# Optimization experiments

Measured on AMD Instinct MI355X. Metric: run time of the kernel, lower is better.

Reference implementation:

```python
import jax, jax.numpy as jnp
import numpy as np

T, B, D, H, O = 64, 64, 512, 512, 128

def setup_inputs() -> dict:
    key = jax.random.key(0)
    ks = jax.random.split(key, 8)
    s = 0.05
    return {
        "x": jax.random.normal(ks[0], (T, B, D), jnp.float32),
        "w_ih": jax.random.normal(ks[1], (T, 4 * H, D), jnp.float32) * s,
        "w_hh": jax.random.normal(ks[2], (T, 4 * H, H), jnp.float32) * s,
        "b_ih": jax.random.normal(ks[3], (T, 4 * H), jnp.float32) * s,
        "b_hh": jax.random.normal(ks[4], (T, 4 * H), jnp.float32) * s,
        "w_ho": jax.random.normal(ks[5], (O, H), jnp.float32) * s,
        "b_ho": jax.random.normal(ks[6], (O,), jnp.float32) * s,
        "lengths": jax.random.randint(ks[7], (B,), 1, T + 1, jnp.int64 if jax.config.jax_enable_x64 else jnp.int32),
    }

def _lstm_scan(x, w_ih, w_hh, b_ih, b_hh):
    bs = x.shape[1]
    h0 = jnp.zeros((bs, H), x.dtype)
    c0 = jnp.zeros((bs, H), x.dtype)

    def step(carry, inp):
        h, c = carry
        xt, Wih, Whh, bih, bhh = inp
        # gates: [B, 4H], torch gate order i, f, g, o
        gates = xt @ Wih.T + bih + h @ Whh.T + bhh
        i, f, g, o = jnp.split(gates, 4, axis=-1)
        c = jax.nn.sigmoid(f) * c + jax.nn.sigmoid(i) * jnp.tanh(g)
        h = jax.nn.sigmoid(o) * jnp.tanh(c)
        return (h, c), h

    (_, _), outs = jax.lax.scan(step, (h0, c0), (x, w_ih, w_hh, b_ih, b_hh))
    return outs  # [T, B, H]

def reference(x, w_ih, w_hh, b_ih, b_hh, w_ho, b_ho, lengths):
    outs = _lstm_scan(x, w_ih, w_hh, b_ih, b_hh)
    bs = x.shape[1]
    h_t = outs[lengths - 1, jnp.arange(bs)]  # [B, H] last valid output per seq
    logits = h_t @ w_ho.T + b_ho
    return jax.nn.log_softmax(logits, axis=1)
```

## Files before the change

### kernel.cpp

```cpp
#include <hip/hip_runtime.h>
#include <math.h>

#define TT 64
#define BB 64
#define DD 512
#define HH 512
#define G4 2048
#define OO 128

typedef unsigned short us16;
typedef __attribute__((ext_vector_type(8))) short bf16x8;
typedef __attribute__((ext_vector_type(4))) float f32x4;
typedef __attribute__((ext_vector_type(4))) unsigned u32x4;

__device__ __forceinline__ unsigned pk_bf16(float lo, float hi) {
  unsigned r;
  asm volatile("v_cvt_pk_bf16_f32 %0, %1, %2" : "=v"(r) : "v"(lo), "v"(hi));
  return r;
}

__device__ __forceinline__ float sigm(float v) { return 1.f / (1.f + expf(-v)); }

__device__ __forceinline__ u32x4 load_b128_cc(const void* p) {
  u32x4 r;
  asm volatile("global_load_dwordx4 %0, %1, off sc0 sc1" : "=v"(r) : "v"(p));
  return r;
}
__device__ __forceinline__ void store_b128_cc(void* p, u32x4 v) {
  asm volatile("global_store_dwordx4 %0, %1, off sc0 sc1" ::"v"(p), "v"(v) : "memory");
}

__global__ __launch_bounds__(256) void phaseA_mfma(
    const float* __restrict__ x, const float* __restrict__ wih,
    const float* __restrict__ bih, const float* __restrict__ bhh,
    float* __restrict__ Gb) {
  __shared__ us16 xa[2][64][64];
  __shared__ us16 wbuf[2][128][64];
  const int tid = threadIdx.x;
  const int t = blockIdx.y;
  const int j0 = blockIdx.x * 128;
  const int wv = tid >> 6, lane = tid & 63;
  const int wm = wv & 1, wn = wv >> 1;
  const float* xb = x + (size_t)t * (BB * DD);
  const float* wg = wih + (size_t)t * (G4 * DD) + (size_t)j0 * DD;

  float4 xr[2][2], wr[4][2];
  int xrow[2], xc[2], wrow[4], wc[4];
#pragma unroll
  for (int i = 0; i < 2; i++) { int cid = tid + i * 256; xrow[i] = cid >> 3; xc[i] = cid & 7; }
#pragma unroll
  for (int i = 0; i < 4; i++) { int cid = tid + i * 256; wrow[i] = cid >> 3; wc[i] = cid & 7; }

  auto loadx = [&](int k0) {
#pragma unroll
    for (int i = 0; i < 2; i++) {
      const float* p = xb + xrow[i] * DD + k0 + xc[i] * 8;
      xr[i][0] = *(const float4*)p; xr[i][1] = *(const float4*)(p + 4);
    }
  };
  auto loadw = [&](int k0) {
#pragma unroll
    for (int i = 0; i < 4; i++) {
      const float* p = wg + (size_t)wrow[i] * DD + k0 + wc[i] * 8;
      wr[i][0] = *(const float4*)p; wr[i][1] = *(const float4*)(p + 4);
    }
  };
  auto store = [&](int buf) {
#pragma unroll
    for (int i = 0; i < 2; i++) {
      uint4 u;
      u.x = pk_bf16(xr[i][0].x, xr[i][0].y); u.y = pk_bf16(xr[i][0].z, xr[i][0].w);
      u.z = pk_bf16(xr[i][1].x, xr[i][1].y); u.w = pk_bf16(xr[i][1].z, xr[i][1].w);
      int p = xc[i] ^ (xrow[i] & 7);
      *(uint4*)&xa[buf][xrow[i]][p * 8] = u;
    }
#pragma unroll
    for (int i = 0; i < 4; i++) {
      uint4 u;
      u.x = pk_bf16(wr[i][0].x, wr[i][0].y); u.y = pk_bf16(wr[i][0].z, wr[i][0].w);
      u.z = pk_bf16(wr[i][1].x, wr[i][1].y); u.w = pk_bf16(wr[i][1].z, wr[i][1].w);
      int p = wc[i] ^ (wrow[i] & 7);
      *(uint4*)&wbuf[buf][wrow[i]][p * 8] = u;
    }
  };

  loadx(0); loadw(0); store(0);
  __syncthreads();

  f32x4 zero = {0.f, 0.f, 0.f, 0.f};
  f32x4 acc[2][4];
#pragma unroll
  for (int mt = 0; mt < 2; mt++)
#pragma unroll
    for (int nt = 0; nt < 4; nt++) acc[mt][nt] = zero;

  for (int s = 0; s < 8; s++) {
    const int nb = s & 1;
    if (s < 7) { loadx((s + 1) * 64); loadw((s + 1) * 64); }
#pragma unroll
    for (int ks = 0; ks < 2; ks++) {
      const int cc = ks * 4 + (lane >> 4);
      bf16x8 a[2], b[4];
#pragma unroll
      for (int mt = 0; mt < 2; mt++) {
        int r = wm * 32 + mt * 16 + (lane & 15);
        a[mt] = *(const bf16x8*)&xa[nb][r][(cc ^ (r & 7)) * 8];
      }
#pragma unroll
      for (int nt = 0; nt < 4; nt++) {
        int r = wn * 64 + nt * 16 + (lane & 15);
        b[nt] = *(const bf16x8*)&wbuf[nb][r][(cc ^ (r & 7)) * 8];
      }
#pragma unroll
      for (int mt = 0; mt < 2; mt++)
#pragma unroll
        for (int nt = 0; nt < 4; nt++)
          acc[mt][nt] = __builtin_amdgcn_mfma_f32_16x16x32_bf16(a[mt], b[nt], acc[mt][nt], 0, 0, 0);
    }
    __syncthreads();
    if (s < 7) store(nb ^ 1);
    __syncthreads();
  }

  float bias[4]; int jn[4];
#pragma unroll
  for (int nt = 0; nt < 4; nt++) {
    jn[nt] = j0 + wn * 64 + nt * 16 + (lane & 15);
    bias[nt] = bih[t * G4 + jn[nt]] + bhh[t * G4 + jn[nt]];
  }
#pragma unroll
  for (int mt = 0; mt < 2; mt++)
#pragma unroll
    for (int nt = 0; nt < 4; nt++)
#pragma unroll
      for (int e = 0; e < 4; e++) {
        int brow = wm * 32 + mt * 16 + (lane >> 4) * 4 + e;
        Gb[((size_t)t * BB + brow) * G4 + jn[nt]] = acc[mt][nt][e] + bias[nt];
      }
}

__global__ __launch_bounds__(256, 1) void lstm_persist(
    const float* __restrict__ whh, const float* __restrict__ Gb,
    const int* __restrict__ lengths, char* __restrict__ hb,
    float* __restrict__ hf) {
  __shared__ float gm[2][16][36];

  const int tid = threadIdx.x, bid = blockIdx.x;
  const int bh = bid & 1, ug = bid >> 1;
  const int wv = tid >> 6, lane = tid & 63;
  const int wm = wv & 1, kq = wv >> 1;
  const int l15 = lane & 15, klg = lane >> 4;

  const size_t jrow = (size_t)((l15 >> 2) * 512 + ug * 4 + (l15 & 3));

  float4 pf[8][2];
  auto prefW = [&](int tt) {
    const float* wt = whh + (size_t)tt * (G4 * HH) + jrow * HH;
#pragma unroll
    for (int s = 0; s < 8; s++) {
      const float* p = wt + (size_t)(kq * 32 + s * 4 + klg) * 8;
      pf[s][0] = *(const float4*)p;
      pf[s][1] = *(const float4*)(p + 4);
    }
  };
  bf16x8 wfrag[8];
  auto cvtW = [&]() {
#pragma unroll
    for (int s = 0; s < 8; s++) {
      uint4 u;
      u.x = pk_bf16(pf[s][0].x, pf[s][0].y); u.y = pk_bf16(pf[s][0].z, pf[s][0].w);
      u.z = pk_bf16(pf[s][1].x, pf[s][1].y); u.w = pk_bf16(pf[s][1].z, pf[s][1].w);
      wfrag[s] = __builtin_bit_cast(bf16x8, u);
    }
  };

  float2 gpre[4];
  auto prefG = [&](int tt) {
    if (wv == 0) {
      const float* gbp =
          Gb + ((size_t)tt * BB + bh * 32 + (lane & 31)) * G4 + ug * 4 + ((lane >> 5) << 1);
#pragma unroll
      for (int q = 0; q < 4; q++) gpre[q] = *(const float2*)(gbp + q * 512);
    }
  };

  const size_t cbase =
      (size_t)bh * 65536 + ((size_t)(kq * 64 + klg * 2) * 32 + wm * 16 + l15) * 16;
  const size_t pbase = (size_t)bh * 65536 + ((size_t)ug * 32 + (lane & 31)) * 16;

  const int mylen = (wv == 0) ? lengths[bh * 32 + (lane & 31)] : -2;
  float cst[2] = {0.f, 0.f};

  prefW(0);
  prefG(0);

  for (int t = 0; t < TT; t++) {
    cvtW();

    u32x4 r0[8], r1[8];
    if (t == 0) {
      u32x4 z = {0u, 0u, 0u, 0u};
#pragma unroll
      for (int s = 0; s < 8; s++) { r0[s] = z; r1[s] = z; }
    } else {
      const char* sbase = hb + (size_t)(t & 1) * 131072 + cbase;
      const unsigned tg = (unsigned)t;
      bool ok;
      do {
#pragma unroll
        for (int s = 0; s < 8; s++) {
          r0[s] = load_b128_cc(sbase + (size_t)s * 4096);
          r1[s] = load_b128_cc(sbase + (size_t)s * 4096 + 512);
        }
        asm volatile("s_waitcnt vmcnt(0)" ::: "memory");
        __builtin_amdgcn_sched_barrier(0);
        ok = true;
#pragma unroll
        for (int s = 0; s < 8; s++) ok = ok && (r0[s].z == tg) && (r1[s].z == tg);
      } while (!__all(ok));
    }

    f32x4 acc = {0.f, 0.f, 0.f, 0.f};
#pragma unroll
    for (int s = 0; s < 8; s++) {
      u32x4 fa;
      fa.x = r0[s].x; fa.y = r0[s].y; fa.z = r1[s].x; fa.w = r1[s].y;
      acc = __builtin_amdgcn_mfma_f32_16x16x32_bf16(__builtin_bit_cast(bf16x8, fa),
                                                    wfrag[s], acc, 0, 0, 0);
    }
    *(f32x4*)&gm[kq][l15][wm * 16 + klg * 4] = acc;

    __syncthreads();

    float2 gcur[4];
    if (wv == 0) {
#pragma unroll
      for (int q = 0; q < 4; q++) gcur[q] = gpre[q];
    }
    if (t + 1 < TT) { prefW(t + 1); prefG(t + 1); }

    if (wv == 0) {
      const int b = lane & 31, hi = lane >> 5;
      float hv[2];
#pragma unroll
      for (int uu = 0; uu < 2; uu++) {
        const int lu = hi * 2 + uu;
        float vi = (uu ? gcur[0].y : gcur[0].x) + gm[0][0 + lu][b] + gm[1][0 + lu][b];
        float vf = (uu ? gcur[1].y : gcur[1].x) + gm[0][4 + lu][b] + gm[1][4 + lu][b];
        float vg = (uu ? gcur[2].y : gcur[2].x) + gm[0][8 + lu][b] + gm[1][8 + lu][b];
        float vo = (uu ? gcur[3].y : gcur[3].x) + gm[0][12 + lu][b] + gm[1][12 + lu][b];
        float cn = sigm(vf) * cst[uu] + sigm(vi) * tanhf(vg);
        cst[uu] = cn;
        hv[uu] = sigm(vo) * tanhf(cn);
      }
      unsigned hw = pk_bf16(hv[0], hv[1]);
      unsigned other = __shfl_xor(hw, 32);
      if (mylen - 1 == t) {
        float2 o2; o2.x = hv[0]; o2.y = hv[1];
        *(float2*)&hf[(size_t)(bh * 32 + b) * HH + ug * 4 + hi * 2] = o2;
      }
      if (hi == 0 && t + 1 < TT) {
        u32x4 rec;
        rec.x = hw; rec.y = other; rec.z = (unsigned)(t + 1); rec.w = 0u;
        store_b128_cc(hb + (size_t)((t + 1) & 1) * 131072 + pbase, rec);
      }
    }
  }
}

__global__ __launch_bounds__(128) void finalK(const float* __restrict__ hf,
                                              const float* __restrict__ who,
                                              const float* __restrict__ bho,
                                              float* __restrict__ out) {
  int b = blockIdx.x, o = threadIdx.x;
  const float* h = hf + b * HH;
  const float* w = who + o * HH;
  float s = bho[o];
#pragma unroll 4
  for (int k = 0; k < HH; k += 4) {
    float4 hv = *(const float4*)(h + k);
    float4 wv = *(const float4*)(w + k);
    s += hv.x * wv.x + hv.y * wv.y + hv.z * wv.z + hv.w * wv.w;
  }
  __shared__ float red[2];
  __shared__ float red2[2];
  float m = s;
#pragma unroll
  for (int msk = 32; msk; msk >>= 1) m = fmaxf(m, __shfl_xor(m, msk));
  int wave = o >> 6;
  if ((o & 63) == 0) red[wave] = m;
  __syncthreads();
  m = fmaxf(red[0], red[1]);
  float e = expf(s - m);
#pragma unroll
  for (int msk = 32; msk; msk >>= 1) e += __shfl_xor(e, msk);
  if ((o & 63) == 0) red2[wave] = e;
  __syncthreads();
  float sum = red2[0] + red2[1];
  out[b * OO + o] = (s - m) - logf(sum);
}

extern "C" void kernel_launch(void* const* d_in, const int* in_sizes, int n_in,
                              void* d_out, int out_size, void* d_ws, size_t ws_size,
                              hipStream_t stream) {
  const float* x = (const float*)d_in[0];
  const float* wih = (const float*)d_in[1];
  const float* whh = (const float*)d_in[2];
  const float* bih = (const float*)d_in[3];
  const float* bhh = (const float*)d_in[4];
  const float* who = (const float*)d_in[5];
  const float* bho = (const float*)d_in[6];
  const int* lengths = (const int*)d_in[7];
  float* out = (float*)d_out;

  char* ws = (char*)d_ws;
  float* Gb = (float*)ws;
  char* hb = ws + 33554432;
  float* hf = (float*)(ws + 33554432 + 262144);

  (void)hipMemsetAsync(hb, 0, 262144, stream);

  phaseA_mfma<<<dim3(16, 64), 256, 0, stream>>>(x, wih, bih, bhh, Gb);
  lstm_persist<<<256, 256, 0, stream>>>(whh, Gb, lengths, hb, hf);
  finalK<<<BB, 128, 0, stream>>>(hf, who, bho, out);
}
```

Measured before the change: 342.9 us.

## Use per-block flags and warp-specialized persistent LSTM with LDS weight staging

Replaces the tagged-payload spin on the whole h buffer with per-block flag words polled by two compute waves. It also splits roles across waves: two waves run the MFMA over the full K, one wave does gate math and publishes h, and one wave prefetches and converts the next step's W_hh into double-buffered swizzled LDS. The goal is to shrink polling traffic and take weight loading off the critical recurrence path. In exchange it adds relaxed-atomic flag ordering that relies on s_waitcnt before the flag store, which carries memory-ordering risk.

```diff
diff --git a/kernel.cpp b/kernel.cpp
--- a/kernel.cpp
+++ b/kernel.cpp
@@ -12,6 +12,7 @@
 typedef __attribute__((ext_vector_type(8))) short bf16x8;
 typedef __attribute__((ext_vector_type(4))) float f32x4;
 typedef __attribute__((ext_vector_type(4))) unsigned u32x4;
+typedef __attribute__((ext_vector_type(2))) unsigned u32x2;
 
 __device__ __forceinline__ unsigned pk_bf16(float lo, float hi) {
   unsigned r;
@@ -26,8 +27,8 @@
   asm volatile("global_load_dwordx4 %0, %1, off sc0 sc1" : "=v"(r) : "v"(p));
   return r;
 }
-__device__ __forceinline__ void store_b128_cc(void* p, u32x4 v) {
-  asm volatile("global_store_dwordx4 %0, %1, off sc0 sc1" ::"v"(p), "v"(v) : "memory");
+__device__ __forceinline__ void store_b64_cc(void* p, u32x2 v) {
+  asm volatile("global_store_dwordx2 %0, %1, off sc0 sc1" ::"v"(p), "v"(v) : "memory");
 }
 
 __global__ __launch_bounds__(256) void phaseA_mfma(
@@ -142,113 +143,91 @@
 __global__ __launch_bounds__(256, 1) void lstm_persist(
     const float* __restrict__ whh, const float* __restrict__ Gb,
     const int* __restrict__ lengths, char* __restrict__ hb,
-    float* __restrict__ hf) {
-  __shared__ float gm[2][16][36];
+    float* __restrict__ hf, unsigned* __restrict__ flags) {
+  __shared__ us16 wbuf[2][16][512];
+  __shared__ float gm[16][36];
 
   const int tid = threadIdx.x, bid = blockIdx.x;
   const int bh = bid & 1, ug = bid >> 1;
   const int wv = tid >> 6, lane = tid & 63;
-  const int wm = wv & 1, kq = wv >> 1;
   const int l15 = lane & 15, klg = lane >> 4;
-
-  const size_t jrow = (size_t)((l15 >> 2) * 512 + ug * 4 + (l15 & 3));
-
-  float4 pf[8][2];
-  auto prefW = [&](int tt) {
-    const float* wt = whh + (size_t)tt * (G4 * HH) + jrow * HH;
-#pragma unroll
-    for (int s = 0; s < 8; s++) {
-      const float* p = wt + (size_t)(kq * 32 + s * 4 + klg) * 8;
-      pf[s][0] = *(const float4*)p;
-      pf[s][1] = *(const float4*)(p + 4);
-    }
-  };
-  bf16x8 wfrag[8];
-  auto cvtW = [&]() {
-#pragma unroll
-    for (int s = 0; s < 8; s++) {
-      uint4 u;
-      u.x = pk_bf16(pf[s][0].x, pf[s][0].y); u.y = pk_bf16(pf[s][0].z, pf[s][0].w);
-      u.z = pk_bf16(pf[s][1].x, pf[s][1].y); u.w = pk_bf16(pf[s][1].z, pf[s][1].w);
-      wfrag[s] = __builtin_bit_cast(bf16x8, u);
-    }
-  };
 
   float2 gpre[4];
   auto prefG = [&](int tt) {
-    if (wv == 0) {
-      const float* gbp =
-          Gb + ((size_t)tt * BB + bh * 32 + (lane & 31)) * G4 + ug * 4 + ((lane >> 5) << 1);
-#pragma unroll
-      for (int q = 0; q < 4; q++) gpre[q] = *(const float2*)(gbp + q * 512);
-    }
+    const float* gbp =
+        Gb + ((size_t)tt * BB + bh * 32 + (lane & 31)) * G4 + ug * 4 + ((lane >> 5) << 1);
+#pragma unroll
+    for (int q = 0; q < 4; q++) gpre[q] = *(const float2*)(gbp + q * 512);
   };
-
-  const size_t cbase =
-      (size_t)bh * 65536 + ((size_t)(kq * 64 + klg * 2) * 32 + wm * 16 + l15) * 16;
-  const size_t pbase = (size_t)bh * 65536 + ((size_t)ug * 32 + (lane & 31)) * 16;
-
-  const int mylen = (wv == 0) ? lengths[bh * 32 + (lane & 31)] : -2;
   float cst[2] = {0.f, 0.f};
-
-  prefW(0);
-  prefG(0);
+  const int mylen = (wv == 2) ? lengths[bh * 32 + (lane & 31)] : -2;
+  if (wv == 2) prefG(0);
+
+  float4 pfA[16], pfB[16];
+
+  const char* crb0 = hb + (size_t)bh * 32768 + (size_t)(wv * 16 + l15) * 1024;
 
   for (int t = 0; t < TT; t++) {
-    cvtW();
-
-    u32x4 r0[8], r1[8];
-    if (t == 0) {
-      u32x4 z = {0u, 0u, 0u, 0u};
-#pragma unroll
-      for (int s = 0; s < 8; s++) { r0[s] = z; r1[s] = z; }
-    } else {
-      const char* sbase = hb + (size_t)(t & 1) * 131072 + cbase;
-      const unsigned tg = (unsigned)t;
-      bool ok;
-      do {
-#pragma unroll
-        for (int s = 0; s < 8; s++) {
-          r0[s] = load_b128_cc(sbase + (size_t)s * 4096);
-          r1[s] = load_b128_cc(sbase + (size_t)s * 4096 + 512);
-        }
-        asm volatile("s_waitcnt vmcnt(0)" ::: "memory");
+    if (wv < 2 && t > 0) {
+      const unsigned tgt = (unsigned)t;
+      const int pidx = (2 * (wv * 64 + lane) + bh) * 4;
+      while (true) {
+        unsigned f = __hip_atomic_load(&flags[pidx], __ATOMIC_RELAXED,
+                                       __HIP_MEMORY_SCOPE_AGENT);
+        if (__all(f >= tgt)) break;
+        __builtin_amdgcn_s_sleep(1);
+      }
+    }
+    __builtin_amdgcn_s_barrier();
+    asm volatile("" ::: "memory");
+
+    if (wv < 2) {
+      f32x4 acc = {0.f, 0.f, 0.f, 0.f};
+      if (t > 0) {
+        const char* rb = crb0 + (size_t)(t & 1) * 65536;
+        u32x4 hfrag[16];
+#pragma unroll
+        for (int s = 0; s < 16; s++)
+          hfrag[s] = load_b128_cc(rb + s * 64 + klg * 16);
+        bf16x8 wf[16];
+#pragma unroll
+        for (int s = 0; s < 16; s++)
+          wf[s] = *(const bf16x8*)&wbuf[t & 1][l15][((4 * s + klg) ^ (l15 & 7)) * 8];
+        asm volatile("s_waitcnt vmcnt(0) lgkmcnt(0)" ::: "memory");
         __builtin_amdgcn_sched_barrier(0);
-        ok = true;
-#pragma unroll
-        for (int s = 0; s < 8; s++) ok = ok && (r0[s].z == tg) && (r1[s].z == tg);
-      } while (!__all(ok));
-    }
-
-    f32x4 acc = {0.f, 0.f, 0.f, 0.f};
-#pragma unroll
-    for (int s = 0; s < 8; s++) {
-      u32x4 fa;
-      fa.x = r0[s].x; fa.y = r0[s].y; fa.z = r1[s].x; fa.w = r1[s].y;
-      acc = __builtin_amdgcn_mfma_f32_16x16x32_bf16(__builtin_bit_cast(bf16x8, fa),
-                                                    wfrag[s], acc, 0, 0, 0);
-    }
-    *(f32x4*)&gm[kq][l15][wm * 16 + klg * 4] = acc;
-
-    __syncthreads();
-
-    float2 gcur[4];
-    if (wv == 0) {
+#pragma unroll
+        for (int s = 0; s < 16; s++)
+          acc = __builtin_amdgcn_mfma_f32_16x16x32_bf16(__builtin_bit_cast(bf16x8, hfrag[s]),
+                                                        wf[s], acc, 0, 0, 0);
+      }
+      *(f32x4*)&gm[l15][wv * 16 + klg * 4] = acc;
+      asm volatile("s_waitcnt lgkmcnt(0)" ::: "memory");
+    }
+    if (wv == 3 && t + 1 < TT) {
+      const float* wt = whh + (size_t)(t + 1) * (G4 * HH);
+#pragma unroll
+      for (int j = 0; j < 16; j++) {
+        const float* p = wt + (size_t)((j >> 2) * 512 + ug * 4 + (j & 3)) * HH + lane * 8;
+        pfA[j] = *(const float4*)p;
+        pfB[j] = *(const float4*)(p + 4);
+      }
+    }
+    __builtin_amdgcn_s_barrier();
+    asm volatile("" ::: "memory");
+
+    if (wv == 2) {
+      float2 gcur[4];
 #pragma unroll
       for (int q = 0; q < 4; q++) gcur[q] = gpre[q];
-    }
-    if (t + 1 < TT) { prefW(t + 1); prefG(t + 1); }
-
-    if (wv == 0) {
       const int b = lane & 31, hi = lane >> 5;
       float hv[2];
 #pragma unroll
       for (int uu = 0; uu < 2; uu++) {
         const int lu = hi * 2 + uu;
-        float vi = (uu ? gcur[0].y : gcur[0].x) + gm[0][0 + lu][b] + gm[1][0 + lu][b];
-        float vf = (uu ? gcur[1].y : gcur[1].x) + gm[0][4 + lu][b] + gm[1][4 + lu][b];
-        float vg = (uu ? gcur[2].y : gcur[2].x) + gm[0][8 + lu][b] + gm[1][8 + lu][b];
-        float vo = (uu ? gcur[3].y : gcur[3].x) + gm[0][12 + lu][b] + gm[1][12 + lu][b];
+        float vi = (uu ? gcur[0].y : gcur[0].x) + gm[0 + lu][b];
+        float vf = (uu ? gcur[1].y : gcur[1].x) + gm[4 + lu][b];
+        float vg = (uu ? gcur[2].y : gcur[2].x) + gm[8 + lu][b];
+        float vo = (uu ? gcur[3].y : gcur[3].x) + gm[12 + lu][b];
         float cn = sigm(vf) * cst[uu] + sigm(vi) * tanhf(vg);
         cst[uu] = cn;
         hv[uu] = sigm(vo) * tanhf(cn);
@@ -259,11 +238,30 @@
         float2 o2; o2.x = hv[0]; o2.y = hv[1];
         *(float2*)&hf[(size_t)(bh * 32 + b) * HH + ug * 4 + hi * 2] = o2;
       }
-      if (hi == 0 && t + 1 < TT) {
-        u32x4 rec;
-        rec.x = hw; rec.y = other; rec.z = (unsigned)(t + 1); rec.w = 0u;
-        store_b128_cc(hb + (size_t)((t + 1) & 1) * 131072 + pbase, rec);
-      }
+      if (t + 1 < TT) {
+        if (lane < 32) {
+          u32x2 rec = {hw, other};
+          store_b64_cc(hb + (size_t)((t + 1) & 1) * 65536 + (size_t)bh * 32768 +
+                           (size_t)(lane * 128 + ug) * 8,
+                       rec);
+        }
+        asm volatile("s_waitcnt vmcnt(0)" ::: "memory");
+        if (lane == 0)
+          __hip_atomic_store(&flags[bid * 4], (unsigned)(t + 1), __ATOMIC_RELAXED,
+                             __HIP_MEMORY_SCOPE_AGENT);
+        prefG(t + 1);
+      }
+    }
+    if (wv == 3 && t + 1 < TT) {
+      const int sl = (t + 1) & 1;
+#pragma unroll
+      for (int j = 0; j < 16; j++) {
+        u32x4 w;
+        w.x = pk_bf16(pfA[j].x, pfA[j].y); w.y = pk_bf16(pfA[j].z, pfA[j].w);
+        w.z = pk_bf16(pfB[j].x, pfB[j].y); w.w = pk_bf16(pfB[j].z, pfB[j].w);
+        *(u32x4*)&wbuf[sl][j][(lane ^ (j & 7)) * 8] = w;
+      }
+      asm volatile("s_waitcnt lgkmcnt(0)" ::: "memory");
     }
   }
 }
@@ -316,11 +314,12 @@
   char* ws = (char*)d_ws;
   float* Gb = (float*)ws;
   char* hb = ws + 33554432;
-  float* hf = (float*)(ws + 33554432 + 262144);
-
-  (void)hipMemsetAsync(hb, 0, 262144, stream);
+  unsigned* flags = (unsigned*)(ws + 33554432 + 131072);
+  float* hf = (float*)(ws + 33554432 + 131072 + 4096);
+
+  (void)hipMemsetAsync(flags, 0, 4096, stream);
 
   phaseA_mfma<<<dim3(16, 64), 256, 0, stream>>>(x, wih, bih, bhh, Gb);
-  lstm_persist<<<256, 256, 0, stream>>>(whh, Gb, lengths, hb, hf);
+  lstm_persist<<<256, 256, 0, stream>>>(whh, Gb, lengths, hb, hf, flags);
   finalK<<<BB, 128, 0, stream>>>(hf, who, bho, out);
 }
```

Measured after the change: 418.2 us. 1.22x slower.

## Split persistent LSTM block into compute and weight-prefetch warp roles

Applied to the files above, without the earlier changes.

Warps 0-1 now each handle the full K=512 reduction for 16 batch rows. They read h from the global exchange buffer and W_hh fragments from a swizzled, double-buffered LDS tile. Warps 2-3 act as producers: they load the next timesteps' fp32 W_hh from global, convert it to bf16, and write it into LDS two steps ahead. This removes the per-step cross-warp partial-sum reduction and takes weight loads off the critical path. In exchange, the gate math and h publish are spread across 128 lanes, and a sleep is added in the spin-wait plus priority hints. The risks are that each compute warp now does twice the MFMA chain length, and that the producer/consumer barrier ordering must stay correct.

```diff
diff --git a/kernel.cpp b/kernel.cpp
--- a/kernel.cpp
+++ b/kernel.cpp
@@ -143,127 +143,124 @@
     const float* __restrict__ whh, const float* __restrict__ Gb,
     const int* __restrict__ lengths, char* __restrict__ hb,
     float* __restrict__ hf) {
-  __shared__ float gm[2][16][36];
+  __shared__ us16 wbuf[2][16][512];
+  __shared__ float gmT[2][16][20];
 
   const int tid = threadIdx.x, bid = blockIdx.x;
   const int bh = bid & 1, ug = bid >> 1;
   const int wv = tid >> 6, lane = tid & 63;
-  const int wm = wv & 1, kq = wv >> 1;
   const int l15 = lane & 15, klg = lane >> 4;
 
-  const size_t jrow = (size_t)((l15 >> 2) * 512 + ug * 4 + (l15 & 3));
-
-  float4 pf[8][2];
-  auto prefW = [&](int tt) {
-    const float* wt = whh + (size_t)tt * (G4 * HH) + jrow * HH;
-#pragma unroll
-    for (int s = 0; s < 8; s++) {
-      const float* p = wt + (size_t)(kq * 32 + s * 4 + klg) * 8;
-      pf[s][0] = *(const float4*)p;
-      pf[s][1] = *(const float4*)(p + 4);
-    }
-  };
-  bf16x8 wfrag[8];
-  auto cvtW = [&]() {
-#pragma unroll
-    for (int s = 0; s < 8; s++) {
-      uint4 u;
-      u.x = pk_bf16(pf[s][0].x, pf[s][0].y); u.y = pk_bf16(pf[s][0].z, pf[s][0].w);
-      u.z = pk_bf16(pf[s][1].x, pf[s][1].y); u.w = pk_bf16(pf[s][1].z, pf[s][1].w);
-      wfrag[s] = __builtin_bit_cast(bf16x8, u);
-    }
-  };
-
-  float2 gpre[4];
-  auto prefG = [&](int tt) {
-    if (wv == 0) {
-      const float* gbp =
-          Gb + ((size_t)tt * BB + bh * 32 + (lane & 31)) * G4 + ug * 4 + ((lane >> 5) << 1);
-#pragma unroll
-      for (int q = 0; q < 4; q++) gpre[q] = *(const float2*)(gbp + q * 512);
-    }
-  };
-
-  const size_t cbase =
-      (size_t)bh * 65536 + ((size_t)(kq * 64 + klg * 2) * 32 + wm * 16 + l15) * 16;
-  const size_t pbase = (size_t)bh * 65536 + ((size_t)ug * 32 + (lane & 31)) * 16;
-
-  const int mylen = (wv == 0) ? lengths[bh * 32 + (lane & 31)] : -2;
-  float cst[2] = {0.f, 0.f};
-
-  prefW(0);
-  prefG(0);
-
-  for (int t = 0; t < TT; t++) {
-    cvtW();
-
-    u32x4 r0[8], r1[8];
-    if (t == 0) {
-      u32x4 z = {0u, 0u, 0u, 0u};
-#pragma unroll
-      for (int s = 0; s < 8; s++) { r0[s] = z; r1[s] = z; }
-    } else {
-      const char* sbase = hb + (size_t)(t & 1) * 131072 + cbase;
-      const unsigned tg = (unsigned)t;
-      bool ok;
-      do {
-#pragma unroll
-        for (int s = 0; s < 8; s++) {
-          r0[s] = load_b128_cc(sbase + (size_t)s * 4096);
-          r1[s] = load_b128_cc(sbase + (size_t)s * 4096 + 512);
+  if (wv < 2) {
+    const int wm = wv;
+    const int bm = bh * 32 + wm * 16 + l15;
+    const int u = l15 & 3;
+    const int ml = klg * 4 + (l15 >> 2);
+    const int bg = bh * 32 + wm * 16 + ml;
+    const int mylen = lengths[bg];
+    float cst = 0.f;
+    const char* crb = hb + (size_t)bm * 2048 + klg * 32;
+
+    for (int t = 0; t < TT; t++) {
+      float g4[4];
+      {
+        const float* gp = Gb + ((size_t)t * BB + bg) * G4 + ug * 4 + u;
+#pragma unroll
+        for (int q = 0; q < 4; q++) g4[q] = gp[q * 512];
+      }
+
+      f32x4 acc = {0.f, 0.f, 0.f, 0.f};
+      if (t > 0) {
+        const char* sb = crb + (size_t)(t & 1) * 131072;
+        const unsigned tg = (unsigned)t;
+        u32x4 ra[16], rb[16];
+        while (true) {
+#pragma unroll
+          for (int s = 0; s < 16; s++) {
+            ra[s] = load_b128_cc(sb + s * 128);
+            rb[s] = load_b128_cc(sb + s * 128 + 16);
+          }
+          asm volatile("s_waitcnt vmcnt(0)" ::: "memory");
+          __builtin_amdgcn_sched_barrier(0);
+          bool ok = true;
+#pragma unroll
+          for (int s = 0; s < 16; s++) ok = ok && (ra[s].z == tg) && (rb[s].z == tg);
+          if (__all(ok)) break;
+          __builtin_amdgcn_s_sleep(1);
         }
-        asm volatile("s_waitcnt vmcnt(0)" ::: "memory");
-        __builtin_amdgcn_sched_barrier(0);
-        ok = true;
-#pragma unroll
-        for (int s = 0; s < 8; s++) ok = ok && (r0[s].z == tg) && (r1[s].z == tg);
-      } while (!__all(ok));
-    }
-
-    f32x4 acc = {0.f, 0.f, 0.f, 0.f};
-#pragma unroll
-    for (int s = 0; s < 8; s++) {
-      u32x4 fa;
-      fa.x = r0[s].x; fa.y = r0[s].y; fa.z = r1[s].x; fa.w = r1[s].y;
-      acc = __builtin_amdgcn_mfma_f32_16x16x32_bf16(__builtin_bit_cast(bf16x8, fa),
-                                                    wfrag[s], acc, 0, 0, 0);
-    }
-    *(f32x4*)&gm[kq][l15][wm * 16 + klg * 4] = acc;
-
-    __syncthreads();
-
-    float2 gcur[4];
-    if (wv == 0) {
-#pragma unroll
-      for (int q = 0; q < 4; q++) gcur[q] = gpre[q];
-    }
-    if (t + 1 < TT) { prefW(t + 1); prefG(t + 1); }
-
-    if (wv == 0) {
-      const int b = lane & 31, hi = lane >> 5;
-      float hv[2];
-#pragma unroll
-      for (int uu = 0; uu < 2; uu++) {
-        const int lu = hi * 2 + uu;
-        float vi = (uu ? gcur[0].y : gcur[0].x) + gm[0][0 + lu][b] + gm[1][0 + lu][b];
-        float vf = (uu ? gcur[1].y : gcur[1].x) + gm[0][4 + lu][b] + gm[1][4 + lu][b];
-        float vg = (uu ? gcur[2].y : gcur[2].x) + gm[0][8 + lu][b] + gm[1][8 + lu][b];
-        float vo = (uu ? gcur[3].y : gcur[3].x) + gm[0][12 + lu][b] + gm[1][12 + lu][b];
-        float cn = sigm(vf) * cst[uu] + sigm(vi) * tanhf(vg);
-        cst[uu] = cn;
-        hv[uu] = sigm(vo) * tanhf(cn);
-      }
-      unsigned hw = pk_bf16(hv[0], hv[1]);
-      unsigned other = __shfl_xor(hw, 32);
-      if (mylen - 1 == t) {
-        float2 o2; o2.x = hv[0]; o2.y = hv[1];
-        *(float2*)&hf[(size_t)(bh * 32 + b) * HH + ug * 4 + hi * 2] = o2;
-      }
-      if (hi == 0 && t + 1 < TT) {
-        u32x4 rec;
-        rec.x = hw; rec.y = other; rec.z = (unsigned)(t + 1); rec.w = 0u;
-        store_b128_cc(hb + (size_t)((t + 1) & 1) * 131072 + pbase, rec);
-      }
+        __builtin_amdgcn_s_setprio(1);
+        bf16x8 wf[16];
+#pragma unroll
+        for (int s = 0; s < 16; s++)
+          wf[s] = *(const bf16x8*)&wbuf[t & 1][l15][((4 * s + klg) ^ (l15 & 7)) * 8];
+        f32x4 a0 = {0.f, 0.f, 0.f, 0.f}, a1 = {0.f, 0.f, 0.f, 0.f};
+#pragma unroll
+        for (int s = 0; s < 16; s++) {
+          u32x4 fa;
+          fa.x = ra[s].x; fa.y = ra[s].y; fa.z = rb[s].x; fa.w = rb[s].y;
+          if (s & 1)
+            a1 = __builtin_amdgcn_mfma_f32_16x16x32_bf16(__builtin_bit_cast(bf16x8, fa), wf[s], a1, 0, 0, 0);
+          else
+            a0 = __builtin_amdgcn_mfma_f32_16x16x32_bf16(__builtin_bit_cast(bf16x8, fa), wf[s], a0, 0, 0, 0);
+        }
+        acc = a0 + a1;
+      }
+
+      *(f32x4*)&gmT[wm][l15][klg * 4] = acc;
+      float vi = g4[0] + gmT[wm][0 + u][ml];
+      float vf = g4[1] + gmT[wm][4 + u][ml];
+      float vg = g4[2] + gmT[wm][8 + u][ml];
+      float vo = g4[3] + gmT[wm][12 + u][ml];
+      float cn = sigm(vf) * cst + sigm(vi) * tanhf(vg);
+      cst = cn;
+      float hv = sigm(vo) * tanhf(cn);
+      if (mylen - 1 == t) hf[(size_t)bg * HH + ug * 4 + u] = hv;
+      if (t + 1 < TT) {
+        float ho = __shfl_xor(hv, 1);
+        unsigned hp = pk_bf16(hv, ho);
+        unsigned hq = __shfl_xor(hp, 2);
+        if (u == 0) {
+          u32x4 rec;
+          rec.x = hp; rec.y = hq; rec.z = (unsigned)(t + 1); rec.w = 0u;
+          store_b128_cc(hb + (size_t)((t + 1) & 1) * 131072 + ((size_t)bg * 128 + ug) * 16, rec);
+        }
+      }
+      __builtin_amdgcn_s_setprio(0);
+      __builtin_amdgcn_s_barrier();
+    }
+  } else {
+    const int jb = (wv - 2) * 8;
+    float4 a0[8], b0[8], a1[8], b1[8];
+    auto issue = [&](int tt, float4* pa, float4* pb) {
+      const float* wt = whh + (size_t)tt * (G4 * HH);
+#pragma unroll
+      for (int j = 0; j < 8; j++) {
+        int jj = jb + j;
+        const float* p = wt + (size_t)((jj >> 2) * 512 + ug * 4 + (jj & 3)) * HH + lane * 8;
+        pa[j] = *(const float4*)p;
+        pb[j] = *(const float4*)(p + 4);
+      }
+    };
+    auto writeL = [&](int sl, float4* pa, float4* pb) {
+#pragma unroll
+      for (int j = 0; j < 8; j++) {
+        int jj = jb + j;
+        u32x4 w;
+        w.x = pk_bf16(pa[j].x, pa[j].y); w.y = pk_bf16(pa[j].z, pa[j].w);
+        w.z = pk_bf16(pb[j].x, pb[j].y); w.w = pk_bf16(pb[j].z, pb[j].w);
+        *(u32x4*)&wbuf[sl][jj][(lane ^ (jj & 7)) * 8] = w;
+      }
+    };
+    issue(1, a0, b0);
+    for (int t = 0; t < TT; t++) {
+      if (t & 1) {
+        if (t + 2 < TT) issue(t + 2, a0, b0);
+        if (t + 1 < TT) writeL((t + 1) & 1, a1, b1);
+      } else {
+        if (t + 2 < TT) issue(t + 2, a1, b1);
+        if (t + 1 < TT) writeL((t + 1) & 1, a0, b0);
+      }
+      __builtin_amdgcn_s_barrier();
     }
   }
 }
```

Result: slower. 468.3 us (+36.6%).
